# Performance work log

Hardware: AMD Instinct MI355X
Metric: run time of the kernel (lower is better)

Reference implementation:

```python
import jax, jax.numpy as jnp
import numpy as np

CUT_SIZE = 224  # cut_size init arg
CUTN = 32       # cutn init arg
CUT_POW = 1.0


def setup_inputs() -> dict:
    key = jax.random.key(0)
    B, C, H, W = 16, 3, 512, 512
    x = jax.random.normal(key, (B, C, H, W), dtype=jnp.float32)
    # Replicate the module's host-side RNG: size = rand()**cut_pow*(max-min)+min,
    # offset = randint(0, side - size + 1). Generated with numpy for determinism.
    rs = np.random.RandomState(0)
    max_size = min(H, W)
    min_size = min(H, W, CUT_SIZE)
    sizes = (rs.rand(CUTN) ** CUT_POW * (max_size - min_size) + min_size).astype(np.int32)
    offsetx = np.floor(rs.rand(CUTN) * (W - sizes + 1)).astype(np.int32)
    offsety = np.floor(rs.rand(CUTN) * (H - sizes + 1)).astype(np.int32)
    return {
        "x": x,
        "sizes": jnp.asarray(sizes),
        "offsetx": jnp.asarray(offsetx),
        "offsety": jnp.asarray(offsety),
    }


def reference(x, sizes, offsetx, offsety):
    # x: [B, C, H, W]; sizes/offsetx/offsety: [cutn] int32
    B, C, H, W = x.shape
    i = jnp.arange(CUT_SIZE, dtype=jnp.int32)
    # PyTorch F.interpolate default 'nearest': src = floor(out_idx * in/out)
    yidx = offsety[:, None] + (i[None, :] * sizes[:, None]) // CUT_SIZE  # [cutn, cut]
    xidx = offsetx[:, None] + (i[None, :] * sizes[:, None]) // CUT_SIZE  # [cutn, cut]
    # Fused crop + nearest-resize for all cutouts via one batched gather
    out = x[:, :, yidx[:, :, None], xidx[:, None, :]]  # [B, C, cutn, cut, cut]
    out = jnp.transpose(out, (2, 0, 1, 3, 4))           # [cutn, B, C, cut, cut]
    return out.reshape(CUTN * B, C, CUT_SIZE, CUT_SIZE)  # matches th.cat over cutn
```

## Files before the change

### kernel.cpp

```cpp
#include <hip/hip_runtime.h>


#define CUT_SIZE 224
#define CUTN     32
#define BATCH    16
#define CHAN     3
#define HEIGHT   512
#define WIDTH    512
#define J4       (CUT_SIZE / 4)

__global__ __launch_bounds__(256) void make_cutouts_kernel(
    const float* __restrict__ x,
    const int*   __restrict__ sizes,
    const int*   __restrict__ offsetx,
    const int*   __restrict__ offsety,
    float4*      __restrict__ out,
    int total_vec4)
{
    int v = blockIdx.x * blockDim.x + threadIdx.x;
    if (v >= total_vec4) return;

    int j4 = v % J4;
    int t  = v / J4;
    int i  = t % CUT_SIZE;
    t /= CUT_SIZE;
    int c  = t % CHAN;
    t /= CHAN;
    int b  = t % BATCH;
    int n  = t / BATCH;

    const int sz = sizes[n];
    const int ox = offsetx[n];
    const int oy = offsety[n];

    const int yy = oy + (i * sz) / CUT_SIZE;
    const int j0 = j4 * 4;
    const int x0 = ox + ((j0 + 0) * sz) / CUT_SIZE;
    const int x1 = ox + ((j0 + 1) * sz) / CUT_SIZE;
    const int x2 = ox + ((j0 + 2) * sz) / CUT_SIZE;
    const int x3 = ox + ((j0 + 3) * sz) / CUT_SIZE;

    const float* __restrict__ row =
        x + ((size_t)((b * CHAN + c) * HEIGHT + yy)) * WIDTH;

    float4 r;
    r.x = row[x0];
    r.y = row[x1];
    r.z = row[x2];
    r.w = row[x3];
    out[v] = r;
}

extern "C" void kernel_launch(void* const* d_in, const int* in_sizes, int n_in,
                              void* d_out, int out_size, void* d_ws, size_t ws_size,
                              hipStream_t stream) {
    const float* x       = (const float*)d_in[0];
    const int*   sizes   = (const int*)d_in[1];
    const int*   offsetx = (const int*)d_in[2];
    const int*   offsety = (const int*)d_in[3];
    float4*      out     = (float4*)d_out;

    const int total_vec4 = CUTN * BATCH * CHAN * CUT_SIZE * J4;
    const int block = 256;
    const int grid  = (total_vec4 + block - 1) / block;

    make_cutouts_kernel<<<grid, block, 0, stream>>>(x, sizes, offsetx, offsety,
                                                    out, total_vec4);
}
```

Measured before the change: 405.2 us.

## Stage source rows into LDS with async global_load_lds triple-buffered pipeline

Each wave now processes a 56-row chunk of one cutout/channel. It asynchronously copies entire source image rows into a 3-deep LDS ring via global_load_lds and gathers the resized columns from LDS. Stores are written as coalesced scalar rows. The aim is to replace scattered global gathers with bulk row loads overlapped with output writes. The cost is reading full 512-wide rows even when crops are narrower, plus manual waitcnt management.

```diff
diff --git a/kernel.cpp b/kernel.cpp
--- a/kernel.cpp
+++ b/kernel.cpp
@@ -7,48 +7,99 @@
 #define CHAN     3
 #define HEIGHT   512
 #define WIDTH    512
-#define J4       (CUT_SIZE / 4)
+#define GROUPS   (CUTN * BATCH * CHAN)
+#define I_PER_WAVE 56
+#define CHUNKS   (CUT_SIZE / I_PER_WAVE)
+#define WPB      4
+#define DEPTH    3
+
+typedef const __attribute__((address_space(1))) void* gas_ptr;
+typedef __attribute__((address_space(3))) void*       las_ptr;
+
+__device__ __forceinline__ void stage_row(const float* src_row, float* lds_buf, int lane)
+{
+    __builtin_amdgcn_global_load_lds((gas_ptr)(src_row + lane * 4),
+                                     (las_ptr)(lds_buf), 16, 0, 0);
+    __builtin_amdgcn_global_load_lds((gas_ptr)(src_row + 256 + lane * 4),
+                                     (las_ptr)(lds_buf + 256), 16, 0, 0);
+}
 
 __global__ __launch_bounds__(256) void make_cutouts_kernel(
     const float* __restrict__ x,
     const int*   __restrict__ sizes,
     const int*   __restrict__ offsetx,
     const int*   __restrict__ offsety,
-    float4*      __restrict__ out,
-    int total_vec4)
+    float*       __restrict__ out)
 {
-    int v = blockIdx.x * blockDim.x + threadIdx.x;
-    if (v >= total_vec4) return;
+    __shared__ __align__(16) float lds[WPB][DEPTH][WIDTH];
 
-    int j4 = v % J4;
-    int t  = v / J4;
-    int i  = t % CUT_SIZE;
-    t /= CUT_SIZE;
-    int c  = t % CHAN;
-    t /= CHAN;
-    int b  = t % BATCH;
-    int n  = t / BATCH;
+    const int wid  = threadIdx.x >> 6;
+    const int lane = threadIdx.x & 63;
+
+    const int task  = blockIdx.x * WPB + wid;
+    const int g     = task >> 2;
+    const int chunk = task & 3;
+
+    const int c  = g % CHAN;
+    const int tb = g / CHAN;
+    const int b  = tb % BATCH;
+    const int n  = tb / BATCH;
 
     const int sz = sizes[n];
     const int ox = offsetx[n];
     const int oy = offsety[n];
 
-    const int yy = oy + (i * sz) / CUT_SIZE;
-    const int j0 = j4 * 4;
-    const int x0 = ox + ((j0 + 0) * sz) / CUT_SIZE;
-    const int x1 = ox + ((j0 + 1) * sz) / CUT_SIZE;
-    const int x2 = ox + ((j0 + 2) * sz) / CUT_SIZE;
-    const int x3 = ox + ((j0 + 3) * sz) / CUT_SIZE;
+    const float* img  = x + (size_t)(b * CHAN + c) * (HEIGHT * WIDTH);
+    float*       outg = out + (size_t)g * (CUT_SIZE * CUT_SIZE)
+                            + (size_t)(chunk * I_PER_WAVE) * CUT_SIZE;
 
-    const float* __restrict__ row =
-        x + ((size_t)((b * CHAN + c) * HEIGHT + yy)) * WIDTH;
+    const unsigned usz = (unsigned)sz;
+    const int xi0 = ox + (int)(((unsigned)(lane      ) * usz) / CUT_SIZE);
+    const int xi1 = ox + (int)(((unsigned)(lane +  64) * usz) / CUT_SIZE);
+    const int xi2 = ox + (int)(((unsigned)(lane + 128) * usz) / CUT_SIZE);
+    const int xi3 = (lane < 32)
+                  ? ox + (int)(((unsigned)(lane + 192) * usz) / CUT_SIZE)
+                  : xi0;
 
-    float4 r;
-    r.x = row[x0];
-    r.y = row[x1];
-    r.z = row[x2];
-    r.w = row[x3];
-    out[v] = r;
+    float* p0 = &lds[wid][0][0];
+    float* p1 = &lds[wid][1][0];
+    float* p2 = &lds[wid][2][0];
+
+    const int ibase = chunk * I_PER_WAVE;
+
+    #define ROW_PTR(K) (img + (size_t)(oy + (int)(((unsigned)((ibase + (K)) * sz)) / CUT_SIZE)) * WIDTH)
+
+    stage_row(ROW_PTR(0), p0, lane);
+    stage_row(ROW_PTR(1), p1, lane);
+    stage_row(ROW_PTR(2), p2, lane);
+
+    for (int k = 0; k < I_PER_WAVE; ++k) {
+        if      (k <  I_PER_WAVE - 2) { asm volatile("s_waitcnt vmcnt(4)" ::: "memory"); }
+        else if (k == I_PER_WAVE - 2) { asm volatile("s_waitcnt vmcnt(2)" ::: "memory"); }
+        else                          { asm volatile("s_waitcnt vmcnt(0)" ::: "memory"); }
+        __builtin_amdgcn_sched_barrier(0);
+
+        const float v0 = p0[xi0];
+        const float v1 = p0[xi1];
+        const float v2 = p0[xi2];
+        const float v3 = p0[xi3];
+
+        asm volatile("s_waitcnt lgkmcnt(0)" ::: "memory");
+        __builtin_amdgcn_sched_barrier(0);
+
+        if (k + DEPTH < I_PER_WAVE) {
+            stage_row(ROW_PTR(k + DEPTH), p0, lane);
+        }
+
+        float* orow = outg + (size_t)k * CUT_SIZE;
+        orow[lane      ] = v0;
+        orow[lane +  64] = v1;
+        orow[lane + 128] = v2;
+        if (lane < 32) orow[lane + 192] = v3;
+
+        float* t = p0; p0 = p1; p1 = p2; p2 = t;
+    }
+    #undef ROW_PTR
 }
 
 extern "C" void kernel_launch(void* const* d_in, const int* in_sizes, int n_in,
@@ -58,12 +109,8 @@
     const int*   sizes   = (const int*)d_in[1];
     const int*   offsetx = (const int*)d_in[2];
     const int*   offsety = (const int*)d_in[3];
-    float4*      out     = (float4*)d_out;
+    float*       out     = (float*)d_out;
 
-    const int total_vec4 = CUTN * BATCH * CHAN * CUT_SIZE * J4;
-    const int block = 256;
-    const int grid  = (total_vec4 + block - 1) / block;
-
-    make_cutouts_kernel<<<grid, block, 0, stream>>>(x, sizes, offsetx, offsety,
-                                                    out, total_vec4);
+    const int grid = GROUPS * CHUNKS / WPB;
+    make_cutouts_kernel<<<grid, 256, 0, stream>>>(x, sizes, offsetx, offsety, out);
 }
```

Result: faster. 394.3 us (-2.7%).
